# Optimization experiments

Hardware: AMD Instinct MI355X
Metric: run time of the kernel (lower is better)

## Reference

```python
import jax, jax.numpy as jnp
import numpy as np

EPS = 1e-5

def _lin(x, w, b):
    return x @ w + b

def _ln(x, scale, bias):
    m = jnp.mean(x, axis=-1, keepdims=True)
    v = jnp.var(x, axis=-1, keepdims=True)
    return (x - m) / jnp.sqrt(v + EPS) * scale + bias

def setup_inputs() -> dict:
    key = jax.random.key(0)
    B, N, F, OUT, TRI = 4, 128, 128, 128, 8
    ks = iter(jax.random.split(key, 64))
    def lin_params(fan_in, fan_out):
        s = 1.0 / np.sqrt(fan_in)
        w = jax.random.uniform(next(ks), (fan_in, fan_out), minval=-s, maxval=s, dtype=jnp.float32)
        b = jax.random.uniform(next(ks), (fan_out,), minval=-s, maxval=s, dtype=jnp.float32)
        return w, b
    inp = {}
    inp['node_fts'] = jax.random.normal(next(ks), (B, N, F), dtype=jnp.float32)
    inp['edge_fts'] = jax.random.normal(next(ks), (B, N, N, F), dtype=jnp.float32)
    inp['graph_fts'] = jax.random.normal(next(ks), (B, F), dtype=jnp.float32)
    inp['hidden'] = jax.random.normal(next(ks), (B, N, F), dtype=jnp.float32)
    inp['adj_matrix'] = jax.random.randint(next(ks), (B, N, N), 0, 2, dtype=jnp.int32)
    inp['m1_w'], inp['m1_b'] = lin_params(2 * F, OUT)
    inp['m2_w'], inp['m2_b'] = lin_params(2 * F, OUT)
    inp['me_w'], inp['me_b'] = lin_params(F, OUT)
    inp['mg_w'], inp['mg_b'] = lin_params(F, OUT)
    inp['mlp1_w'], inp['mlp1_b'] = lin_params(OUT, OUT)
    inp['mlp2_w'], inp['mlp2_b'] = lin_params(OUT, OUT)
    inp['o1_w'], inp['o1_b'] = lin_params(2 * F, OUT)
    inp['o2_w'], inp['o2_b'] = lin_params(OUT, OUT)
    inp['t1_w'], inp['t1_b'] = lin_params(2 * F, TRI)
    inp['t2_w'], inp['t2_b'] = lin_params(2 * F, TRI)
    inp['te1_w'], inp['te1_b'] = lin_params(F, TRI)
    inp['te2_w'], inp['te2_b'] = lin_params(F, TRI)
    inp['te3_w'], inp['te3_b'] = lin_params(F, TRI)
    inp['tg_w'], inp['tg_b'] = lin_params(F, TRI)
    inp['o3_w'], inp['o3_b'] = lin_params(TRI, OUT)
    inp['norm_scale'] = jnp.ones((OUT,), dtype=jnp.float32)
    inp['norm_bias'] = jnp.zeros((OUT,), dtype=jnp.float32)
    return inp

def reference(node_fts, edge_fts, graph_fts, hidden, adj_matrix,
              m1_w, m1_b, m2_w, m2_b, me_w, me_b, mg_w, mg_b,
              mlp1_w, mlp1_b, mlp2_w, mlp2_b,
              o1_w, o1_b, o2_w, o2_b,
              t1_w, t1_b, t2_w, t2_b,
              te1_w, te1_b, te2_w, te2_b, te3_w, te3_b,
              tg_w, tg_b, o3_w, o3_b, norm_scale, norm_bias):
    z = jnp.concatenate([node_fts, hidden], axis=-1)          # [B,N,2F]
    msg_1 = _lin(z, m1_w, m1_b)                                # [B,N,H]
    msg_2 = _lin(z, m2_w, m2_b)
    msg_e = _lin(edge_fts, me_w, me_b)                         # [B,N,N,H]
    msg_g = _lin(graph_fts, mg_w, mg_b)                        # [B,H]
    msgs = msg_1[:, None, :, :] + msg_2[:, :, None, :] + msg_e + msg_g[:, None, None, :]
    # msg_mlp: ReLU -> Linear -> ReLU -> Linear
    msgs = _lin(jax.nn.relu(_lin(jax.nn.relu(msgs), mlp1_w, mlp1_b)), mlp2_w, mlp2_b)
    # triplet messages (note: original code reuses t_1 for tri_3 -- faithful)
    tri_1 = _lin(z, t1_w, t1_b)                                # [B,N,T]
    tri_2 = _lin(z, t2_w, t2_b)
    tri_3 = _lin(z, t1_w, t1_b)
    tri_e_1 = _lin(edge_fts, te1_w, te1_b)                     # [B,N,N,T]
    tri_e_2 = _lin(edge_fts, te2_w, te2_b)
    tri_e_3 = _lin(edge_fts, te3_w, te3_b)
    tri_g = _lin(graph_fts, tg_w, tg_b)                        # [B,T]
    triplets = (tri_1[:, :, None, None, :] + tri_2[:, None, :, None, :]
                + tri_3[:, None, None, :, :]
                + tri_e_1[:, :, :, None, :] + tri_e_2[:, :, None, :, :]
                + tri_e_3[:, None, :, :, :]
                + tri_g[:, None, None, None, :])               # [B,N,N,N,T]
    tri_msgs = _lin(jnp.max(triplets, axis=1), o3_w, o3_b)     # [B,N,N,OUT]
    tri_msgs = _ln(jax.nn.relu(tri_msgs), norm_scale, norm_bias)
    # masked max aggregation
    maxarg = jnp.where(adj_matrix[..., None] == 1, msgs, -1e9)
    msgs_agg = jnp.max(maxarg, axis=1)                         # [B,N,H]
    out = jax.nn.relu(_lin(z, o1_w, o1_b) + _lin(msgs_agg, o2_w, o2_b))
    out = _ln(out, norm_scale, norm_bias)
    return out, tri_msgs
```

## Files before the change

kernel.cpp:

```cpp
#include <hip/hip_runtime.h>
#include <hip/hip_bf16.h>
#include <cstddef>
#include <cstdint>
#include <cstring>

typedef __attribute__((ext_vector_type(8))) short bf16x8;
typedef __attribute__((ext_vector_type(4))) float f32x4;
typedef unsigned short ushort_t;

__device__ __forceinline__ ushort_t f2b(float f) {
    uint32_t x = __float_as_uint(f);
    uint32_t r = (x + 0x7FFFu + ((x >> 16) & 1u)) >> 16;
    return (ushort_t)r;
}
__device__ __forceinline__ float b2f(ushort_t u) {
    return __uint_as_float(((uint32_t)u) << 16);
}
__device__ __forceinline__ uint32_t pk2(float x, float y) {
    __hip_bfloat162 h = __float22bfloat162_rn(float2{x, y});
    uint32_t u;
    __builtin_memcpy(&u, &h, 4);
    return u;
}

__global__ void prep_kernel(const float* __restrict__ m1_w, const float* __restrict__ m2_w,
                            const float* __restrict__ o1_w, const float* __restrict__ t1_w,
                            const float* __restrict__ t2_w,
                            const float* __restrict__ me_w, const float* __restrict__ mlp1_w,
                            const float* __restrict__ mlp2_w,
                            const float* __restrict__ te1_w, const float* __restrict__ te2_w,
                            const float* __restrict__ te3_w,
                            const float* __restrict__ graph_fts,
                            const float* __restrict__ mg_w, const float* __restrict__ mg_b,
                            const float* __restrict__ m1_b,
                            const float* __restrict__ tg_w, const float* __restrict__ t2_b,
                            const float* __restrict__ tg_b,
                            ushort_t* __restrict__ Wnt,
                            ushort_t* __restrict__ Wme, ushort_t* __restrict__ Wm1,
                            ushort_t* __restrict__ Wm2, ushort_t* __restrict__ TEt,
                            float* __restrict__ G1, float* __restrict__ TG) {
    int idx = blockIdx.x * 256 + threadIdx.x;
    if (idx < 106496) {
        int o = idx >> 8, k = idx & 255;
        float v = 0.0f;
        if (o < 128)       v = m1_w[k * 128 + o];
        else if (o < 256)  v = m2_w[k * 128 + (o - 128)];
        else if (o < 384)  v = o1_w[k * 128 + (o - 256)];
        else if (o < 392)  v = t1_w[k * 8 + (o - 384)];
        else if (o < 400)  v = t2_w[k * 8 + (o - 392)];
        Wnt[idx] = f2b(v);
    } else if (idx < 122880) {
        int t = idx - 106496, o = t >> 7, h = t & 127;
        Wme[t] = f2b(me_w[h * 128 + o]);
    } else if (idx < 139264) {
        int t = idx - 122880, o = t >> 7, h = t & 127;
        Wm1[t] = f2b(mlp1_w[h * 128 + o]);
    } else if (idx < 155648) {
        int t = idx - 139264, o = t >> 7, h = t & 127;
        Wm2[t] = f2b(mlp2_w[h * 128 + o]);
    } else if (idx < 159744) {
        int t = idx - 155648, c = t >> 7, h = t & 127;
        float v = 0.0f;
        if (c < 8)       v = te1_w[h * 8 + c];
        else if (c < 16) v = te2_w[h * 8 + (c - 8)];
        else if (c < 24) v = te3_w[h * 8 + (c - 16)];
        TEt[t] = f2b(v);
    } else if (idx < 160256) {
        int t = idx - 159744, b = t >> 7, h = t & 127;
        float a = m1_b[h] + mg_b[h];
        #pragma unroll 4
        for (int k = 0; k < 128; k++) a = fmaf(graph_fts[b * 128 + k], mg_w[k * 128 + h], a);
        G1[t] = a;
    } else if (idx < 160288) {
        int t = idx - 160256, b = t >> 3, tt = t & 7;
        float a = t2_b[tt] + tg_b[tt];
        #pragma unroll 4
        for (int k = 0; k < 128; k++) a = fmaf(graph_fts[b * 128 + k], tg_w[k * 8 + tt], a);
        TG[t] = a;
    }
}

__global__ __launch_bounds__(256)
void node_gemm(const float* __restrict__ node_fts, const float* __restrict__ hidden,
               const ushort_t* __restrict__ Wnt,
               const float* __restrict__ G1, const float* __restrict__ m2_b,
               const float* __restrict__ o1_b, const float* __restrict__ t1_b,
               const float* __restrict__ TG,
               float* __restrict__ M1, float* __restrict__ M2, float* __restrict__ O1z,
               float* __restrict__ T1v, float* __restrict__ TT2) {
    __shared__ ushort_t Zs[32 * 256];
    char* Zb = (char*)Zs;
    const int tid = threadIdx.x;
    const int blk = blockIdx.x;
    const int rowblk = blk >> 1, colh = blk & 1;
    const int b = rowblk >> 2, q = rowblk & 3;
    const int row0 = b * 128 + q * 32;
    const int w = tid >> 6, l = tid & 63, g = l >> 4, lq = l & 15;

    const float4* nsrc = reinterpret_cast<const float4*>(node_fts + (size_t)row0 * 128);
    const float4* hsrc = reinterpret_cast<const float4*>(hidden + (size_t)row0 * 128);
    #pragma unroll
    for (int p = 0; p < 8; p++) {
        int idx = tid + p * 256;
        int r = idx >> 6, c4 = idx & 63;
        float4 v = (c4 < 32) ? nsrc[r * 32 + c4] : hsrc[r * 32 + (c4 - 32)];
        uint2 pk;
        pk.x = pk2(v.x, v.y);
        pk.y = pk2(v.z, v.w);
        *reinterpret_cast<uint2*>(Zb + r * 512 + (((c4 >> 1) ^ (r & 7)) << 4) + (c4 & 1) * 8) = pk;
    }
    __syncthreads();

    for (int mt = colh * 13 + w; mt < colh * 13 + 13; mt += 4) {
        f32x4 acc0 = (f32x4){0.f, 0.f, 0.f, 0.f};
        f32x4 acc1 = (f32x4){0.f, 0.f, 0.f, 0.f};
        const ushort_t* arow = Wnt + (size_t)(mt * 16 + lq) * 256;
        #pragma unroll
        for (int ks = 0; ks < 8; ks++) {
            bf16x8 a = *reinterpret_cast<const bf16x8*>(arow + ks * 32 + g * 8);
            int j0 = lq, j1 = 16 + lq;
            bf16x8 b0 = *reinterpret_cast<const bf16x8*>(Zb + j0 * 512 + (((ks * 4 + g) ^ (j0 & 7)) << 4));
            bf16x8 b1 = *reinterpret_cast<const bf16x8*>(Zb + j1 * 512 + (((ks * 4 + g) ^ (j1 & 7)) << 4));
            acc0 = __builtin_amdgcn_mfma_f32_16x16x32_bf16(a, b0, acc0, 0, 0, 0);
            acc1 = __builtin_amdgcn_mfma_f32_16x16x32_bf16(a, b1, acc1, 0, 0, 0);
        }
        #pragma unroll
        for (int half = 0; half < 2; half++) {
            const f32x4 acc = half ? acc1 : acc0;
            const int grow = row0 + half * 16 + lq;
            #pragma unroll
            for (int c = 0; c < 4; c++) {
                int o = mt * 16 + g * 4 + c;
                float v = acc[c];
                if (o < 128)       M1[(size_t)grow * 128 + o] = v + G1[b * 128 + o];
                else if (o < 256)  M2[(size_t)grow * 128 + (o - 128)] = v + m2_b[o - 128];
                else if (o < 384)  O1z[(size_t)grow * 128 + (o - 256)] = v + o1_b[o - 256];
                else if (o < 392)  T1v[(size_t)grow * 8 + (o - 384)] = v + t1_b[o - 384];
                else if (o < 400)  TT2[(size_t)grow * 8 + (o - 392)] = v + TG[b * 8 + (o - 392)];
            }
        }
    }
}

__device__ __forceinline__ void mmv(const ushort_t* __restrict__ Wt, const char* Xa,
                                    f32x4 acc[2][4], int o_blk, int j_blk, int g, int lq) {
    #pragma unroll
    for (int ks = 0; ks < 4; ks++) {
        bf16x8 a[2], bb[4];
        #pragma unroll
        for (int m = 0; m < 2; m++)
            a[m] = *reinterpret_cast<const bf16x8*>(Wt + (size_t)(o_blk + m * 16 + lq) * 128 + ks * 32 + g * 8);
        #pragma unroll
        for (int n = 0; n < 4; n++) {
            int j = j_blk + n * 16 + lq;
            bb[n] = *reinterpret_cast<const bf16x8*>(Xa + j * 256 + (((ks * 4 + g) ^ (j & 7)) << 4));
        }
        #pragma unroll
        for (int m = 0; m < 2; m++)
            #pragma unroll
            for (int n = 0; n < 4; n++)
                acc[m][n] = __builtin_amdgcn_mfma_f32_16x16x32_bf16(a[m], bb[n], acc[m][n], 0, 0, 0);
    }
}

__global__ __launch_bounds__(512, 4)
void edge_kernel(const float* __restrict__ edge_fts,
                 const ushort_t* __restrict__ Wme, const float* __restrict__ me_b,
                 const ushort_t* __restrict__ Wm1, const float* __restrict__ mlp1_b,
                 const ushort_t* __restrict__ Wm2, const float* __restrict__ mlp2_b,
                 const ushort_t* __restrict__ TEt,
                 const float* __restrict__ te1_b, const float* __restrict__ te2_b,
                 const float* __restrict__ te3_b,
                 const float* __restrict__ M1,  const float* __restrict__ M2,
                 const float* __restrict__ T1v, const float* __restrict__ TT2,
                 const int* __restrict__ adj, const float* __restrict__ O1z,
                 const float* __restrict__ o2_w, const float* __restrict__ o2_b,
                 const float* __restrict__ nsc, const float* __restrict__ nbi,
                 float* __restrict__ out,
                 ushort_t* __restrict__ T1buf, ushort_t* __restrict__ T2buf,
                 ushort_t* __restrict__ E3buf) {
    __shared__ ushort_t Xs[2][16384];
    char* X0 = (char*)Xs[0];
    char* X1 = (char*)Xs[1];
    const int tid = threadIdx.x;
    const int b  = blockIdx.x >> 7;
    const int jf = blockIdx.x & 127;
    const int w = tid >> 6, l = tid & 63, g = l >> 4, lq = l & 15;
    const int o_blk = (w & 3) * 32, j_blk = (w >> 2) * 64;

    #pragma unroll
    for (int p = 0; p < 8; p++) {
        int idx = tid + p * 512;
        int r = idx >> 5, c4 = idx & 31;
        const float4* src = reinterpret_cast<const float4*>(
            edge_fts + ((size_t)(b * 128 + r) * 128 + jf) * 128);
        float4 v = src[c4];
        uint2 pk;
        pk.x = pk2(v.x, v.y);
        pk.y = pk2(v.z, v.w);
        *reinterpret_cast<uint2*>(X0 + r * 256 + (((c4 >> 1) ^ (r & 7)) << 4) + (c4 & 1) * 8) = pk;
    }
    __syncthreads();

    uint2 tsvA[2];
    uint2 tsvB[2];
    const int m_te = w & 1;
    const int jq = (w >> 1) & 3;
    {
        const ushort_t* At = TEt + m_te * 16 * 128;
        f32x4 acc2[2];
        #pragma unroll
        for (int n = 0; n < 2; n++) acc2[n] = (f32x4){0.f, 0.f, 0.f, 0.f};
        #pragma unroll
        for (int ks = 0; ks < 4; ks++) {
            bf16x8 a = *reinterpret_cast<const bf16x8*>(At + lq * 128 + ks * 32 + g * 8);
            #pragma unroll
            for (int n = 0; n < 2; n++) {
                int j = jq * 32 + n * 16 + lq;
                bf16x8 bbv = *reinterpret_cast<const bf16x8*>(X0 + j * 256 + (((ks * 4 + g) ^ (j & 7)) << 4));
                acc2[n] = __builtin_amdgcn_mfma_f32_16x16x32_bf16(a, bbv, acc2[n], 0, 0, 0);
            }
        }
        if (m_te == 0) {
            if (g < 2) {
                int t0 = g * 4;
                const float4 eb = *reinterpret_cast<const float4*>(te1_b + t0);
                #pragma unroll
                for (int n = 0; n < 2; n++) {
                    int r = jq * 32 + n * 16 + lq;
                    const float4 tv = *reinterpret_cast<const float4*>(T1v + (size_t)(b * 128 + r) * 8 + t0);
                    tsvA[n].x = pk2(acc2[n][0] + eb.x + tv.x, acc2[n][1] + eb.y + tv.y);
                    tsvA[n].y = pk2(acc2[n][2] + eb.z + tv.z, acc2[n][3] + eb.w + tv.w);
                }
            } else {
                int t0 = g * 4 - 8;
                const float4 eb = *reinterpret_cast<const float4*>(te2_b + t0);
                #pragma unroll
                for (int n = 0; n < 2; n++) {
                    tsvA[n].x = pk2(acc2[n][0] + eb.x, acc2[n][1] + eb.y);
                    tsvA[n].y = pk2(acc2[n][2] + eb.z, acc2[n][3] + eb.w);
                }
            }
        } else if (g < 2) {
            int t0 = g * 4;
            const float4 eb = *reinterpret_cast<const float4*>(te3_b + t0);
            const float4 t3v = *reinterpret_cast<const float4*>(T1v + (size_t)(b * 128 + jf) * 8 + t0);
            #pragma unroll
            for (int n = 0; n < 2; n++) {
                int r = jq * 32 + n * 16 + lq;
                const float4 t2v = *reinterpret_cast<const float4*>(TT2 + (size_t)(b * 128 + r) * 8 + t0);
                tsvB[n].x = pk2(acc2[n][0] + eb.x + t2v.x + t3v.x, acc2[n][1] + eb.y + t2v.y + t3v.y);
                tsvB[n].y = pk2(acc2[n][2] + eb.z + t2v.z + t3v.z, acc2[n][3] + eb.w + t2v.w + t3v.w);
            }
        }
    }

    f32x4 acc[2][4];

    #pragma unroll
    for (int m = 0; m < 2; m++)
        #pragma unroll
        for (int n = 0; n < 4; n++) acc[m][n] = (f32x4){0.f, 0.f, 0.f, 0.f};
    mmv(Wme, X0, acc, o_blk, j_blk, g, lq);
    {
        #pragma unroll
        for (int m = 0; m < 2; m++) {
            int o0 = o_blk + m * 16 + g * 4;
            const float4 eb = *reinterpret_cast<const float4*>(me_b + o0);
            const float4 m1 = *reinterpret_cast<const float4*>(M1 + (size_t)(b * 128 + jf) * 128 + o0);
            float4 bc = make_float4(eb.x + m1.x, eb.y + m1.y, eb.z + m1.z, eb.w + m1.w);
            #pragma unroll
            for (int n = 0; n < 4; n++) {
                int j = j_blk + n * 16 + lq;
                const float4 m2 = *reinterpret_cast<const float4*>(M2 + (size_t)(b * 128 + j) * 128 + o0);
                float r0 = fmaxf(acc[m][n][0] + bc.x + m2.x, 0.f);
                float r1 = fmaxf(acc[m][n][1] + bc.y + m2.y, 0.f);
                float r2 = fmaxf(acc[m][n][2] + bc.z + m2.z, 0.f);
                float r3 = fmaxf(acc[m][n][3] + bc.w + m2.w, 0.f);
                uint2 pk;
                pk.x = pk2(r0, r1);
                pk.y = pk2(r2, r3);
                *reinterpret_cast<uint2*>(X1 + j * 256 + ((((o0 >> 3) ^ (j & 7))) << 4) + (o0 & 7) * 2) = pk;
            }
        }
        __syncthreads();
    }

    #pragma unroll
    for (int m = 0; m < 2; m++)
        #pragma unroll
        for (int n = 0; n < 4; n++) acc[m][n] = (f32x4){0.f, 0.f, 0.f, 0.f};
    mmv(Wm1, X1, acc, o_blk, j_blk, g, lq);
    {
        #pragma unroll
        for (int m = 0; m < 2; m++) {
            int o0 = o_blk + m * 16 + g * 4;
            const float4 bb = *reinterpret_cast<const float4*>(mlp1_b + o0);
            #pragma unroll
            for (int n = 0; n < 4; n++) {
                int j = j_blk + n * 16 + lq;
                float r0 = fmaxf(acc[m][n][0] + bb.x, 0.f);
                float r1 = fmaxf(acc[m][n][1] + bb.y, 0.f);
                float r2 = fmaxf(acc[m][n][2] + bb.z, 0.f);
                float r3 = fmaxf(acc[m][n][3] + bb.w, 0.f);
                uint2 pk;
                pk.x = pk2(r0, r1);
                pk.y = pk2(r2, r3);
                *reinterpret_cast<uint2*>(X0 + j * 256 + ((((o0 >> 3) ^ (j & 7))) << 4) + (o0 & 7) * 2) = pk;
            }
        }
        __syncthreads();
    }

    #pragma unroll
    for (int m = 0; m < 2; m++)
        #pragma unroll
        for (int n = 0; n < 4; n++) acc[m][n] = (f32x4){0.f, 0.f, 0.f, 0.f};
    mmv(Wm2, X0, acc, o_blk, j_blk, g, lq);
    {
        #pragma unroll
        for (int m = 0; m < 2; m++) {
            int o0 = o_blk + m * 16 + g * 4;
            const float4 bb = *reinterpret_cast<const float4*>(mlp2_b + o0);
            #pragma unroll
            for (int n = 0; n < 4; n++) {
                int j = j_blk + n * 16 + lq;
                float r0 = acc[m][n][0] + bb.x;
                float r1 = acc[m][n][1] + bb.y;
                float r2 = acc[m][n][2] + bb.z;
                float r3 = acc[m][n][3] + bb.w;
                uint2 pk;
                pk.x = pk2(r0, r1);
                pk.y = pk2(r2, r3);
                *reinterpret_cast<uint2*>(X1 + j * 256 + ((((o0 >> 3) ^ (j & 7))) << 4) + (o0 & 7) * 2) = pk;
            }
        }
        __syncthreads();
    }

    {
        if (m_te == 0) {
            if (g < 2) {
                int t0 = g * 4;
                #pragma unroll
                for (int n = 0; n < 2; n++) {
                    int r = jq * 32 + n * 16 + lq;
                    *reinterpret_cast<uint2*>(T1buf + ((size_t)(b * 128 + jf) * 128 + r) * 8 + t0) = tsvA[n];
                }
            } else {
                int t0 = g * 4 - 8;
                #pragma unroll
                for (int n = 0; n < 2; n++) {
                    int r = jq * 32 + n * 16 + lq;
                    *reinterpret_cast<uint2*>(T2buf + ((size_t)(b * 128 + r) * 128 + jf) * 8 + t0) = tsvA[n];
                }
            }
        } else if (g < 2) {
            int t0 = g * 4;
            #pragma unroll
            for (int n = 0; n < 2; n++) {
                int r = jq * 32 + n * 16 + lq;
                *reinterpret_cast<uint2*>(E3buf + ((size_t)(b * 128 + r) * 128 + jf) * 8 + t0) = tsvB[n];
            }
        }
    }

    {
        float* scr  = reinterpret_cast<float*>(X0);
        float* aggs = scr;
        float* fagg = scr + 512;
        float* sums = scr + 640;
        const int h = tid & 127, wv = tid >> 7;
        float o1zv0 = 0.f, o1zv1 = 0.f, ob0 = 0.f, ob1 = 0.f;
        float sc0 = 0.f, sc1 = 0.f, bi0 = 0.f, bi1 = 0.f;
        if (w == 0) {
            const float* o1p = O1z + (size_t)(b * 128 + jf) * 128;
            o1zv0 = o1p[l];      o1zv1 = o1p[l + 64];
            ob0 = o2_b[l];       ob1 = o2_b[l + 64];
            sc0 = nsc[l];        sc1 = nsc[l + 64];
            bi0 = nbi[l];        bi1 = nbi[l + 64];
        }
        {
            const int* acol = adj + b * 16384 + jf;
            float amax = -1e9f;
            #pragma unroll 8
            for (int s = 0; s < 32; s++) {
                int r = wv * 32 + s;
                ushort_t u = *reinterpret_cast<const ushort_t*>(
                    X1 + r * 256 + (((h >> 3) ^ (r & 7)) << 4) + (h & 7) * 2);
                amax = (acol[r * 128] == 1) ? fmaxf(amax, b2f(u)) : amax;
            }
            aggs[wv * 128 + h] = amax;
        }
        __syncthreads();
        if (tid < 128)
            fagg[tid] = fmaxf(fmaxf(aggs[tid], aggs[128 + tid]),
                              fmaxf(aggs[256 + tid], aggs[384 + tid]));
        __syncthreads();
        {
            float part = 0.f;
            const float* wcol = o2_w + h;
            #pragma unroll 8
            for (int k = wv * 32; k < wv * 32 + 32; k++)
                part = fmaf(fagg[k], wcol[k * 128], part);
            sums[wv * 128 + h] = part;
        }
        __syncthreads();
        if (w == 0) {
            float v0 = fmaxf(ob0 + o1zv0 + sums[l] + sums[128 + l] + sums[256 + l] + sums[384 + l], 0.f);
            float v1 = fmaxf(ob1 + o1zv1 + sums[l + 64] + sums[128 + l + 64] + sums[256 + l + 64] + sums[384 + l + 64], 0.f);
            float s = v0 + v1, s2 = v0 * v0 + v1 * v1;
            #pragma unroll
            for (int off = 32; off >= 1; off >>= 1) {
                s  += __shfl_xor(s, off, 64);
                s2 += __shfl_xor(s2, off, 64);
            }
            const float mean = s * (1.0f / 128.0f);
            const float var = s2 * (1.0f / 128.0f) - mean * mean;
            const float rstd = rsqrtf(var + 1e-5f);
            float* dst = out + (size_t)(b * 128 + jf) * 128;
            dst[l]      = (v0 - mean) * rstd * sc0 + bi0;
            dst[l + 64] = (v1 - mean) * rstd * sc1 + bi1;
        }
    }
}

__global__ __launch_bounds__(512)
void tri_kernel(const ushort_t* __restrict__ T1buf, const ushort_t* __restrict__ T2buf,
                const ushort_t* __restrict__ E3buf, const float* __restrict__ o3_w,
                const float* __restrict__ o3_b, const float* __restrict__ scale,
                const float* __restrict__ bias, float* __restrict__ tri_out) {
    __shared__ __align__(16) float T1s[1024];
    __shared__ __align__(16) float E3s[1024];
    __shared__ __align__(16) float o3s[1024];
    __shared__ __align__(16) float Ps[4][128][8];
    const int b = blockIdx.x >> 7, jf = blockIdx.x & 127;
    const int tid = threadIdx.x;
    if (tid < 128) {
        uint4 u = reinterpret_cast<const uint4*>(T1buf + (size_t)(b * 128 + jf) * 1024)[tid];
        float* d = &T1s[tid * 8];
        d[0] = b2f((ushort_t)u.x); d[1] = b2f((ushort_t)(u.x >> 16));
        d[2] = b2f((ushort_t)u.y); d[3] = b2f((ushort_t)(u.y >> 16));
        d[4] = b2f((ushort_t)u.z); d[5] = b2f((ushort_t)(u.z >> 16));
        d[6] = b2f((ushort_t)u.w); d[7] = b2f((ushort_t)(u.w >> 16));
    } else if (tid < 256) {
        int t = tid - 128;
        uint4 u = reinterpret_cast<const uint4*>(E3buf + (size_t)(b * 128 + jf) * 1024)[t];
        float* d = &E3s[t * 8];
        d[0] = b2f((ushort_t)u.x); d[1] = b2f((ushort_t)(u.x >> 16));
        d[2] = b2f((ushort_t)u.y); d[3] = b2f((ushort_t)(u.y >> 16));
        d[4] = b2f((ushort_t)u.z); d[5] = b2f((ushort_t)(u.z >> 16));
        d[6] = b2f((ushort_t)u.w); d[7] = b2f((ushort_t)(u.w >> 16));
    } else {
        int t = tid - 256;
        reinterpret_cast<float4*>(o3s)[t] = reinterpret_cast<const float4*>(o3_w)[t];
    }
    __syncthreads();

    {
        const int kf = tid & 127, ih = tid >> 7;
        float a8[8];
        #pragma unroll
        for (int t = 0; t < 8; t++) a8[t] = -3.0e38f;
        const uint4* t2p = reinterpret_cast<const uint4*>(T2buf + (size_t)b * 131072);
        #pragma unroll 4
        for (int ii = 0; ii < 32; ++ii) {
            const int i = ih * 32 + ii;
            uint4 u = t2p[i * 128 + kf];
            const float* t1r = &T1s[i * 8];
            a8[0] = fmaxf(a8[0], t1r[0] + b2f((ushort_t)u.x));
            a8[1] = fmaxf(a8[1], t1r[1] + b2f((ushort_t)(u.x >> 16)));
            a8[2] = fmaxf(a8[2], t1r[2] + b2f((ushort_t)u.y));
            a8[3] = fmaxf(a8[3], t1r[3] + b2f((ushort_t)(u.y >> 16)));
            a8[4] = fmaxf(a8[4], t1r[4] + b2f((ushort_t)u.z));
            a8[5] = fmaxf(a8[5], t1r[5] + b2f((ushort_t)(u.z >> 16)));
            a8[6] = fmaxf(a8[6], t1r[6] + b2f((ushort_t)u.w));
            a8[7] = fmaxf(a8[7], t1r[7] + b2f((ushort_t)(u.w >> 16)));
        }
        #pragma unroll
        for (int t = 0; t < 8; t++) Ps[ih][kf][t] = a8[t];
    }
    __syncthreads();

    const int w = tid >> 6, l = tid & 63;
    const float ob0 = o3_b[l],     ob1 = o3_b[l + 64];
    const float sc0 = scale[l],    sc1 = scale[l + 64];
    const float bi0 = bias[l],     bi1 = bias[l + 64];
    for (int kk = 0; kk < 16; ++kk) {
        const int kf = w * 16 + kk;
        float m8[8];
        #pragma unroll
        for (int t = 0; t < 8; t++)
            m8[t] = fmaxf(fmaxf(Ps[0][kf][t], Ps[1][kf][t]),
                          fmaxf(Ps[2][kf][t], Ps[3][kf][t])) + E3s[kf * 8 + t];
        float v0 = ob0, v1 = ob1;
        #pragma unroll
        for (int t = 0; t < 8; t++) {
            v0 = fmaf(m8[t], o3s[t * 128 + l], v0);
            v1 = fmaf(m8[t], o3s[t * 128 + l + 64], v1);
        }
        v0 = fmaxf(v0, 0.0f);
        v1 = fmaxf(v1, 0.0f);
        float s = v0 + v1, s2 = v0 * v0 + v1 * v1;
        #pragma unroll
        for (int off = 32; off >= 1; off >>= 1) {
            s  += __shfl_xor(s, off, 64);
            s2 += __shfl_xor(s2, off, 64);
        }
        const float mean = s * (1.0f / 128.0f);
        const float var = s2 * (1.0f / 128.0f) - mean * mean;
        const float rstd = rsqrtf(var + 1e-5f);
        float* dst = tri_out + (size_t)((b * 128 + jf) * 128 + kf) * 128;
        dst[l]      = (v0 - mean) * rstd * sc0 + bi0;
        dst[l + 64] = (v1 - mean) * rstd * sc1 + bi1;
    }
}

extern "C" void kernel_launch(void* const* d_in, const int* in_sizes, int n_in,
                              void* d_out, int out_size, void* d_ws, size_t ws_size,
                              hipStream_t stream) {
    const float* node_fts  = (const float*)d_in[0];
    const float* edge_fts  = (const float*)d_in[1];
    const float* graph_fts = (const float*)d_in[2];
    const float* hidden    = (const float*)d_in[3];
    const int*   adj       = (const int*)d_in[4];
    const float* m1_w = (const float*)d_in[5],  *m1_b = (const float*)d_in[6];
    const float* m2_w = (const float*)d_in[7],  *m2_b = (const float*)d_in[8];
    const float* me_w = (const float*)d_in[9],  *me_b = (const float*)d_in[10];
    const float* mg_w = (const float*)d_in[11], *mg_b = (const float*)d_in[12];
    const float* mlp1_w = (const float*)d_in[13], *mlp1_b = (const float*)d_in[14];
    const float* mlp2_w = (const float*)d_in[15], *mlp2_b = (const float*)d_in[16];
    const float* o1_w = (const float*)d_in[17], *o1_b = (const float*)d_in[18];
    const float* o2_w = (const float*)d_in[19], *o2_b = (const float*)d_in[20];
    const float* t1_w = (const float*)d_in[21], *t1_b = (const float*)d_in[22];
    const float* t2_w = (const float*)d_in[23], *t2_b = (const float*)d_in[24];
    const float* te1_w = (const float*)d_in[25], *te1_b = (const float*)d_in[26];
    const float* te2_w = (const float*)d_in[27], *te2_b = (const float*)d_in[28];
    const float* te3_w = (const float*)d_in[29], *te3_b = (const float*)d_in[30];
    const float* tg_w = (const float*)d_in[31], *tg_b = (const float*)d_in[32];
    const float* o3_w = (const float*)d_in[33], *o3_b = (const float*)d_in[34];
    const float* norm_scale = (const float*)d_in[35];
    const float* norm_bias  = (const float*)d_in[36];

    char* w8 = (char*)d_ws;
    float*    M1    = (float*)(w8 + 0);
    float*    M2    = (float*)(w8 + 262144);
    float*    O1z   = (float*)(w8 + 524288);
    float*    T1v   = (float*)(w8 + 786432);
    float*    TT2   = (float*)(w8 + 802816);
    ushort_t* Wme   = (ushort_t*)(w8 + 819200);
    ushort_t* Wm1   = (ushort_t*)(w8 + 851968);
    ushort_t* Wm2   = (ushort_t*)(w8 + 884736);
    ushort_t* TEt   = (ushort_t*)(w8 + 917504);
    ushort_t* T1buf = (ushort_t*)(w8 + 17702912);
    ushort_t* T2buf = (ushort_t*)(w8 + 19800064);
    ushort_t* E3buf = (ushort_t*)(w8 + 21897216);
    ushort_t* Wnt   = (ushort_t*)(w8 + 23994368);
    float*    G1    = (float*)(w8 + 24207360);
    float*    TG    = (float*)(w8 + 24209408);

    float* out_p  = (float*)d_out;
    float* tri_p  = (float*)d_out + 65536;

    prep_kernel<<<627, 256, 0, stream>>>(m1_w, m2_w, o1_w, t1_w, t2_w,
                                         me_w, mlp1_w, mlp2_w, te1_w, te2_w, te3_w,
                                         graph_fts, mg_w, mg_b, m1_b, tg_w, t2_b, tg_b,
                                         Wnt, Wme, Wm1, Wm2, TEt, G1, TG);
    node_gemm<<<32, 256, 0, stream>>>(node_fts, hidden, Wnt, G1, m2_b, o1_b, t1_b, TG,
                                      M1, M2, O1z, T1v, TT2);
    edge_kernel<<<512, 512, 0, stream>>>(edge_fts, Wme, me_b, Wm1, mlp1_b, Wm2, mlp2_b,
                                         TEt, te1_b, te2_b, te3_b,
                                         M1, M2, T1v, TT2,
                                         adj, O1z, o2_w, o2_b, norm_scale, norm_bias,
                                         out_p, T1buf, T2buf, E3buf);
    tri_kernel<<<512, 512, 0, stream>>>(T1buf, T2buf, E3buf, o3_w, o3_b,
                                        norm_scale, norm_bias, tri_p);
}
```

Baseline: 90.62 us.

## Split tri_kernel over k halves and prefetch edge epilogue operands early

tri_kernel now launches twice as many blocks, each handling half the k range. The i-reduction is spread over 8 partial slices of 16 rows instead of 4 of 32, which raises parallelism across the GPU's compute units. In edge_kernel, the adjacency column and the o2_w column slice are loaded into shared memory and registers at kernel start, along with the O1z, bias and norm values. This hides their global-load latency behind the main GEMM work and removes one barrier from the aggregation epilogue. The trade-off is 32 more registers per thread in a kernel with launch bounds of 512 threads and 4 blocks, and the T1 and o3 loads are now duplicated across the two half blocks.

```diff
diff --git a/kernel.cpp b/kernel.cpp
--- a/kernel.cpp
+++ b/kernel.cpp
@@ -180,6 +180,7 @@
                  ushort_t* __restrict__ T1buf, ushort_t* __restrict__ T2buf,
                  ushort_t* __restrict__ E3buf) {
     __shared__ ushort_t Xs[2][16384];
+    __shared__ int adjs[128];
     char* X0 = (char*)Xs[0];
     char* X1 = (char*)Xs[1];
     const int tid = threadIdx.x;
@@ -187,6 +188,22 @@
     const int jf = blockIdx.x & 127;
     const int w = tid >> 6, l = tid & 63, g = l >> 4, lq = l & 15;
     const int o_blk = (w & 3) * 32, j_blk = (w >> 2) * 64;
+    const int h = tid & 127, wv = tid >> 7;
+
+    if (tid < 128) adjs[tid] = adj[b * 16384 + jf + tid * 128];
+    float wreg[32];
+    #pragma unroll
+    for (int s = 0; s < 32; s++)
+        wreg[s] = o2_w[(size_t)(wv * 32 + s) * 128 + h];
+    float o1zv0 = 0.f, o1zv1 = 0.f, ob0 = 0.f, ob1 = 0.f;
+    float sc0 = 0.f, sc1 = 0.f, bi0 = 0.f, bi1 = 0.f;
+    if (w == 0) {
+        const float* o1p = O1z + (size_t)(b * 128 + jf) * 128;
+        o1zv0 = o1p[l];      o1zv1 = o1p[l + 64];
+        ob0 = o2_b[l];       ob1 = o2_b[l + 64];
+        sc0 = nsc[l];        sc1 = nsc[l + 64];
+        bi0 = nbi[l];        bi1 = nbi[l + 64];
+    }
 
     #pragma unroll
     for (int p = 0; p < 8; p++) {
@@ -368,41 +385,28 @@
     {
         float* scr  = reinterpret_cast<float*>(X0);
         float* aggs = scr;
-        float* fagg = scr + 512;
-        float* sums = scr + 640;
-        const int h = tid & 127, wv = tid >> 7;
-        float o1zv0 = 0.f, o1zv1 = 0.f, ob0 = 0.f, ob1 = 0.f;
-        float sc0 = 0.f, sc1 = 0.f, bi0 = 0.f, bi1 = 0.f;
-        if (w == 0) {
-            const float* o1p = O1z + (size_t)(b * 128 + jf) * 128;
-            o1zv0 = o1p[l];      o1zv1 = o1p[l + 64];
-            ob0 = o2_b[l];       ob1 = o2_b[l + 64];
-            sc0 = nsc[l];        sc1 = nsc[l + 64];
-            bi0 = nbi[l];        bi1 = nbi[l + 64];
-        }
+        float* sums = scr + 512;
         {
-            const int* acol = adj + b * 16384 + jf;
             float amax = -1e9f;
             #pragma unroll 8
             for (int s = 0; s < 32; s++) {
                 int r = wv * 32 + s;
                 ushort_t u = *reinterpret_cast<const ushort_t*>(
                     X1 + r * 256 + (((h >> 3) ^ (r & 7)) << 4) + (h & 7) * 2);
-                amax = (acol[r * 128] == 1) ? fmaxf(amax, b2f(u)) : amax;
+                amax = (adjs[r] == 1) ? fmaxf(amax, b2f(u)) : amax;
             }
             aggs[wv * 128 + h] = amax;
         }
-        __syncthreads();
-        if (tid < 128)
-            fagg[tid] = fmaxf(fmaxf(aggs[tid], aggs[128 + tid]),
-                              fmaxf(aggs[256 + tid], aggs[384 + tid]));
         __syncthreads();
         {
             float part = 0.f;
-            const float* wcol = o2_w + h;
-            #pragma unroll 8
-            for (int k = wv * 32; k < wv * 32 + 32; k++)
-                part = fmaf(fagg[k], wcol[k * 128], part);
+            #pragma unroll
+            for (int s = 0; s < 32; s++) {
+                int k = wv * 32 + s;
+                float mk = fmaxf(fmaxf(aggs[k], aggs[128 + k]),
+                                 fmaxf(aggs[256 + k], aggs[384 + k]));
+                part = fmaf(mk, wreg[s], part);
+            }
             sums[wv * 128 + h] = part;
         }
         __syncthreads();
@@ -431,10 +435,12 @@
                 const float* __restrict__ o3_b, const float* __restrict__ scale,
                 const float* __restrict__ bias, float* __restrict__ tri_out) {
     __shared__ __align__(16) float T1s[1024];
-    __shared__ __align__(16) float E3s[1024];
+    __shared__ __align__(16) float E3s[512];
     __shared__ __align__(16) float o3s[1024];
-    __shared__ __align__(16) float Ps[4][128][8];
-    const int b = blockIdx.x >> 7, jf = blockIdx.x & 127;
+    __shared__ __align__(16) float Ps[8][64][8];
+    const int blk = blockIdx.x;
+    const int b = blk >> 8, jf = (blk >> 1) & 127, kh = blk & 1;
+    const int kf0 = kh * 64;
     const int tid = threadIdx.x;
     if (tid < 128) {
         uint4 u = reinterpret_cast<const uint4*>(T1buf + (size_t)(b * 128 + jf) * 1024)[tid];
@@ -443,29 +449,30 @@
         d[2] = b2f((ushort_t)u.y); d[3] = b2f((ushort_t)(u.y >> 16));
         d[4] = b2f((ushort_t)u.z); d[5] = b2f((ushort_t)(u.z >> 16));
         d[6] = b2f((ushort_t)u.w); d[7] = b2f((ushort_t)(u.w >> 16));
-    } else if (tid < 256) {
+    } else if (tid < 192) {
         int t = tid - 128;
-        uint4 u = reinterpret_cast<const uint4*>(E3buf + (size_t)(b * 128 + jf) * 1024)[t];
+        uint4 u = reinterpret_cast<const uint4*>(E3buf + (size_t)(b * 128 + jf) * 1024)[kf0 + t];
         float* d = &E3s[t * 8];
         d[0] = b2f((ushort_t)u.x); d[1] = b2f((ushort_t)(u.x >> 16));
         d[2] = b2f((ushort_t)u.y); d[3] = b2f((ushort_t)(u.y >> 16));
         d[4] = b2f((ushort_t)u.z); d[5] = b2f((ushort_t)(u.z >> 16));
         d[6] = b2f((ushort_t)u.w); d[7] = b2f((ushort_t)(u.w >> 16));
-    } else {
+    } else if (tid >= 256) {
         int t = tid - 256;
         reinterpret_cast<float4*>(o3s)[t] = reinterpret_cast<const float4*>(o3_w)[t];
     }
     __syncthreads();
 
     {
-        const int kf = tid & 127, ih = tid >> 7;
+        const int kfl = tid & 63, ih = tid >> 6;
+        const int kf = kf0 + kfl;
         float a8[8];
         #pragma unroll
         for (int t = 0; t < 8; t++) a8[t] = -3.0e38f;
         const uint4* t2p = reinterpret_cast<const uint4*>(T2buf + (size_t)b * 131072);
         #pragma unroll 4
-        for (int ii = 0; ii < 32; ++ii) {
-            const int i = ih * 32 + ii;
+        for (int ii = 0; ii < 16; ++ii) {
+            const int i = ih * 16 + ii;
             uint4 u = t2p[i * 128 + kf];
             const float* t1r = &T1s[i * 8];
             a8[0] = fmaxf(a8[0], t1r[0] + b2f((ushort_t)u.x));
@@ -478,7 +485,7 @@
             a8[7] = fmaxf(a8[7], t1r[7] + b2f((ushort_t)(u.w >> 16)));
         }
         #pragma unroll
-        for (int t = 0; t < 8; t++) Ps[ih][kf][t] = a8[t];
+        for (int t = 0; t < 8; t++) Ps[ih][kfl][t] = a8[t];
     }
     __syncthreads();
 
@@ -486,13 +493,17 @@
     const float ob0 = o3_b[l],     ob1 = o3_b[l + 64];
     const float sc0 = scale[l],    sc1 = scale[l + 64];
     const float bi0 = bias[l],     bi1 = bias[l + 64];
-    for (int kk = 0; kk < 16; ++kk) {
-        const int kf = w * 16 + kk;
+    for (int kk = 0; kk < 8; ++kk) {
+        const int kfl = w * 8 + kk;
         float m8[8];
         #pragma unroll
-        for (int t = 0; t < 8; t++)
-            m8[t] = fmaxf(fmaxf(Ps[0][kf][t], Ps[1][kf][t]),
-                          fmaxf(Ps[2][kf][t], Ps[3][kf][t])) + E3s[kf * 8 + t];
+        for (int t = 0; t < 8; t++) {
+            float m01 = fmaxf(Ps[0][kfl][t], Ps[1][kfl][t]);
+            float m23 = fmaxf(Ps[2][kfl][t], Ps[3][kfl][t]);
+            float m45 = fmaxf(Ps[4][kfl][t], Ps[5][kfl][t]);
+            float m67 = fmaxf(Ps[6][kfl][t], Ps[7][kfl][t]);
+            m8[t] = fmaxf(fmaxf(m01, m23), fmaxf(m45, m67)) + E3s[kfl * 8 + t];
+        }
         float v0 = ob0, v1 = ob1;
         #pragma unroll
         for (int t = 0; t < 8; t++) {
@@ -510,7 +521,7 @@
         const float mean = s * (1.0f / 128.0f);
         const float var = s2 * (1.0f / 128.0f) - mean * mean;
         const float rstd = rsqrtf(var + 1e-5f);
-        float* dst = tri_out + (size_t)((b * 128 + jf) * 128 + kf) * 128;
+        float* dst = tri_out + (size_t)((b * 128 + jf) * 128 + kf0 + kfl) * 128;
         dst[l]      = (v0 - mean) * rstd * sc0 + bi0;
         dst[l + 64] = (v1 - mean) * rstd * sc1 + bi1;
     }
@@ -573,6 +584,6 @@
                                          M1, M2, T1v, TT2,
                                          adj, O1z, o2_w, o2_b, norm_scale, norm_bias,
                                          out_p, T1buf, T2buf, E3buf);
-    tri_kernel<<<512, 512, 0, stream>>>(T1buf, T2buf, E3buf, o3_w, o3_b,
-                                        norm_scale, norm_bias, tri_p);
-}
+    tri_kernel<<<1024, 512, 0, stream>>>(T1buf, T2buf, E3buf, o3_w, o3_b,
+                                         norm_scale, norm_bias, tri_p);
+}
```

Measured after the change: 94.24 us. +4.0%, slower.
